# Kernel tuning notes

Hardware: AMD Instinct MI355X
Metric: run time of the kernel (lower is better)

Reference implementation:

```python
import math
import jax, jax.numpy as jnp
import numpy as np

CUTOFF = 5.0
NUM_RADIAL = 8   # num_basis_features
L_IN = 3         # basis_max_degree
L_OUT = 4        # moment_max_degree
F_OUT = 64       # num_moment_features


def _fact(n):
    return float(math.factorial(int(n)))


def _cg_complex(j1, j2, j3):
    """Clebsch-Gordan coefficients <j1 m1 j2 m2 | j3 m3> (Racah formula), complex SH basis."""
    C = np.zeros((2 * j1 + 1, 2 * j2 + 1, 2 * j3 + 1))
    for m1 in range(-j1, j1 + 1):
        for m2 in range(-j2, j2 + 1):
            m3 = m1 + m2
            if abs(m3) > j3:
                continue
            pref = math.sqrt((2 * j3 + 1) * _fact(j1 + j2 - j3) * _fact(j1 - j2 + j3)
                             * _fact(-j1 + j2 + j3) / _fact(j1 + j2 + j3 + 1))
            pref *= math.sqrt(_fact(j1 + m1) * _fact(j1 - m1) * _fact(j2 + m2)
                              * _fact(j2 - m2) * _fact(j3 + m3) * _fact(j3 - m3))
            kmin = max(0, j2 - j3 - m1, j1 - j3 + m2)
            kmax = min(j1 + j2 - j3, j1 - m1, j2 + m2)
            s = 0.0
            for k in range(kmin, kmax + 1):
                s += (-1) ** k / (_fact(k) * _fact(j1 + j2 - j3 - k) * _fact(j1 - m1 - k)
                                  * _fact(j2 + m2 - k) * _fact(j3 - j2 + m1 + k) * _fact(j3 - j1 - m2 + k))
            C[m1 + j1, m2 + j2, m3 + j3] = pref * s
    return C


def _u(l):
    """Unitary map complex SH -> real SH, m ordered -l..l."""
    U = np.zeros((2 * l + 1, 2 * l + 1), dtype=np.complex128)
    U[l, l] = 1.0
    for m in range(1, l + 1):
        U[l + m, l + m] = (-1) ** m / math.sqrt(2)
        U[l + m, l - m] = 1.0 / math.sqrt(2)
        U[l - m, l + m] = -1j * (-1) ** m / math.sqrt(2)
        U[l - m, l - m] = 1j / math.sqrt(2)
    return U


def _real_cg(l1, l2, l3):
    C = np.einsum('ai,bj,ck,ijk->abc', _u(l1), _u(l2), np.conj(_u(l3)), _cg_complex(l1, l2, l3))
    # parity-even paths (l1+l2+l3 even) are purely real in the real-SH basis
    return np.real(C).astype(np.float32)


# allowed coupling paths: triangle inequality + proper-tensor parity selection rule
PATHS = [(l1, l2, l3) for l1 in range(L_IN + 1) for l2 in range(L_IN + 1)
         for l3 in range(L_OUT + 1)
         if abs(l1 - l2) <= l3 <= l1 + l2 and (l1 + l2 + l3) % 2 == 0]
CG = {p: jnp.asarray(_real_cg(*p)) for p in PATHS}
OFF_IN = [0, 1, 4, 9, 16]  # degree-block offsets for max_degree=3


def _sph16(u):
    """Real orthonormal spherical harmonics l=0..3 on unit vectors, m=-l..l ordering."""
    x, y, z = u[..., 0], u[..., 1], u[..., 2]
    x2, y2, z2 = x * x, y * y, z * z
    Y = [
        0.28209479177387814 * jnp.ones_like(x),
        0.4886025119029199 * y, 0.4886025119029199 * z, 0.4886025119029199 * x,
        1.0925484305920792 * x * y, 1.0925484305920792 * y * z,
        0.31539156525252005 * (3.0 * z2 - 1.0),
        1.0925484305920792 * x * z, 0.5462742152960396 * (x2 - y2),
        0.5900435899266435 * y * (3.0 * x2 - y2), 2.890611442640554 * x * y * z,
        0.4570457994644658 * y * (5.0 * z2 - 1.0), 0.3731763325901154 * z * (5.0 * z2 - 3.0),
        0.4570457994644658 * x * (5.0 * z2 - 1.0), 1.445305721320277 * z * (x2 - y2),
        0.5900435899266435 * x * (x2 - 3.0 * y2),
    ]
    return jnp.stack(Y, axis=-1)


def _forward(disp, W1, W2):
    # disp: (N, M, 3)
    r = jnp.sqrt(jnp.sum(disp * disp, axis=-1) + 1e-12)          # (N, M)
    u = disp / r[..., None]
    Yang = _sph16(u)                                             # (N, M, 16)
    n = jnp.arange(1, NUM_RADIAL + 1, dtype=disp.dtype)
    radial = jnp.sinc(n * (r[..., None] / CUTOFF))               # sinc radial basis (N, M, 8)
    s2 = jnp.square(r / CUTOFF)
    inside = s2 < 1.0
    cut = jnp.where(inside, jnp.exp(1.0 - 1.0 / (1.0 - jnp.where(inside, s2, 0.0))), 0.0)
    basis = Yang[..., :, None] * (radial * cut[..., None])[..., None, :]   # (N, M, 16, 8)
    # TensorDense: two per-degree dense branches, then Clebsch-Gordan coupling
    y1 = [jnp.einsum('...mf,fg->...mg', basis[..., OFF_IN[l]:OFF_IN[l + 1], :], W1[l]) for l in range(L_IN + 1)]
    y2 = [jnp.einsum('...mf,fg->...mg', basis[..., OFF_IN[l]:OFF_IN[l + 1], :], W2[l]) for l in range(L_IN + 1)]
    out = [jnp.zeros(r.shape + (2 * l3 + 1, F_OUT), disp.dtype) for l3 in range(L_OUT + 1)]
    for (l1, l2, l3) in PATHS:
        out[l3] = out[l3] + jnp.einsum('...if,...jf,ijk->...kf', y1[l1], y2[l2], CG[(l1, l2, l3)])
    return jnp.concatenate(out, axis=-2)                         # (N, M, 25, 64)


def setup_inputs():
    key = jax.random.key(0)
    k1, k2, k3 = jax.random.split(key, 3)
    disp = 2.0 * jax.random.normal(k1, (4096, 16, 3), dtype=jnp.float32)
    W1 = jax.random.normal(k2, (4, 8, 64), dtype=jnp.float32) / math.sqrt(8.0)
    W2 = jax.random.normal(k3, (4, 8, 64), dtype=jnp.float32) / math.sqrt(8.0)
    return {"neighbour_displacements": disp, "W1": W1, "W2": W2}


def reference(neighbour_displacements, W1, W2):
    return _forward(neighbour_displacements, W1, W2)
```

## Files before the change

### kernel.cpp

```cpp
#include <hip/hip_runtime.h>
#include <cmath>
#include <complex>
#include <vector>
#include <algorithm>
#include <cstring>


#define MAXNNZ 4096

struct CGTab {
  int   rowPtr[136];
  int   ij[MAXNNZ];
  float co[MAXNNZ];
};

__device__ CGTab d_tab;


static double factd(int n) { double f = 1.0; for (int i = 2; i <= n; ++i) f *= (double)i; return f; }

static void cg_complex(int j1, int j2, int j3, std::vector<double>& C) {
  int d2 = 2 * j2 + 1, d3 = 2 * j3 + 1;
  C.assign((2 * j1 + 1) * d2 * d3, 0.0);
  for (int m1 = -j1; m1 <= j1; ++m1)
    for (int m2 = -j2; m2 <= j2; ++m2) {
      int m3 = m1 + m2;
      if (m3 < -j3 || m3 > j3) continue;
      double pref = std::sqrt((2 * j3 + 1) * factd(j1 + j2 - j3) * factd(j1 - j2 + j3) *
                              factd(-j1 + j2 + j3) / factd(j1 + j2 + j3 + 1));
      pref *= std::sqrt(factd(j1 + m1) * factd(j1 - m1) * factd(j2 + m2) *
                        factd(j2 - m2) * factd(j3 + m3) * factd(j3 - m3));
      int kmin = std::max(0, std::max(j2 - j3 - m1, j1 - j3 + m2));
      int kmax = std::min(j1 + j2 - j3, std::min(j1 - m1, j2 + m2));
      double s = 0.0;
      for (int k = kmin; k <= kmax; ++k) {
        s += ((k & 1) ? -1.0 : 1.0) /
             (factd(k) * factd(j1 + j2 - j3 - k) * factd(j1 - m1 - k) *
              factd(j2 + m2 - k) * factd(j3 - j2 + m1 + k) * factd(j3 - j1 - m2 + k));
      }
      C[((m1 + j1) * d2 + (m2 + j2)) * d3 + (m3 + j3)] = pref * s;
    }
}

static void umat(int l, std::vector<std::complex<double>>& U) {
  int d = 2 * l + 1;
  U.assign(d * d, std::complex<double>(0, 0));
  U[l * d + l] = 1.0;
  const double is2 = 1.0 / std::sqrt(2.0);
  for (int m = 1; m <= l; ++m) {
    double sg = (m & 1) ? -1.0 : 1.0;
    U[(l + m) * d + (l + m)] = sg * is2;
    U[(l + m) * d + (l - m)] = is2;
    U[(l - m) * d + (l + m)] = std::complex<double>(0, -sg * is2);
    U[(l - m) * d + (l - m)] = std::complex<double>(0, is2);
  }
}

static void real_cg(int l1, int l2, int l3, std::vector<double>& R) {
  std::vector<double> Cc;
  cg_complex(l1, l2, l3, Cc);
  std::vector<std::complex<double>> U1, U2, U3;
  umat(l1, U1); umat(l2, U2); umat(l3, U3);
  int d1 = 2 * l1 + 1, d2 = 2 * l2 + 1, d3 = 2 * l3 + 1;
  R.assign(d1 * d2 * d3, 0.0);
  for (int a = 0; a < d1; ++a)
    for (int b = 0; b < d2; ++b)
      for (int c = 0; c < d3; ++c) {
        std::complex<double> s(0, 0);
        for (int i = 0; i < d1; ++i)
          for (int j = 0; j < d2; ++j) {
            int k = (i - l1) + (j - l2) + l3;
            if (k < 0 || k >= d3) continue;
            double cc = Cc[(i * d2 + j) * d3 + k];
            if (cc == 0.0) continue;
            s += U1[a * d1 + i] * U2[b * d2 + j] * std::conj(U3[c * d3 + k]) * cc;
          }
        R[(a * d2 + b) * d3 + c] = s.real();
      }
}

static void build_tab(CGTab& T) {
  static const int off_in[5] = {0, 1, 4, 9, 16};
  int nnz = 0, slot = 0;
  std::vector<double> R;
  for (int l1 = 0; l1 <= 3; ++l1)
    for (int l2 = 0; l2 <= 3; ++l2)
      for (int l3 = 0; l3 <= 4; ++l3) {
        if (!(std::abs(l1 - l2) <= l3 && l3 <= l1 + l2 && ((l1 + l2 + l3) % 2 == 0))) continue;
        real_cg(l1, l2, l3, R);
        int d2 = 2 * l2 + 1, d3 = 2 * l3 + 1;
        for (int c = 0; c < d3; ++c) {
          T.rowPtr[slot] = nnz;
          for (int a = 0; a < 2 * l1 + 1; ++a)
            for (int b = 0; b < d2; ++b) {
              double v = R[(a * d2 + b) * d3 + c];
              if (std::fabs(v) > 1e-8 && nnz < MAXNNZ) {
                T.ij[nnz] = (off_in[l1] + a) | ((off_in[l2] + b) << 8);
                T.co[nnz] = (float)v;
                ++nnz;
              }
            }
          ++slot;
        }
      }
  T.rowPtr[slot] = nnz;
}


#define OUT_OFF(l3) ((l3) == 0 ? 0 : ((l3) == 1 ? 1 : ((l3) == 2 ? 4 : ((l3) == 3 ? 9 : 16))))

#define PATH(l1, l2, l3, sb)                                        \
  {                                                                 \
    const float t = R1v[l1] * R2v[l2];                              \
    _Pragma("unroll")                                               \
    for (int k = 0; k < 2 * (l3) + 1; ++k)                          \
      o[OUT_OFF(l3) + k] += t * Pl[(sb) + k];                       \
  }

__global__ __launch_bounds__(256) void atmd_kernel(
    const float* __restrict__ disp, const float* __restrict__ W1,
    const float* __restrict__ W2, float* __restrict__ out, int nE) {
  __shared__ float Ysh[4][16];
  __shared__ float P[4][136];

  const int tid = threadIdx.x;
  const int eL = tid >> 6;
  const int f = tid & 63;
  const int e = blockIdx.x * 4 + eL;
  const int ec = e < nE ? e : nE - 1;

  const float dx = disp[3 * ec + 0], dy = disp[3 * ec + 1], dz = disp[3 * ec + 2];
  const float r = sqrtf(dx * dx + dy * dy + dz * dz + 1e-12f);
  const float rinv = 1.0f / r;
  const float x = dx * rinv, y = dy * rinv, z = dz * rinv;
  const float x2 = x * x, y2 = y * y, z2 = z * z;

  const float s = r * 0.2f;
  const float s2 = s * s;
  const float cut = (s2 < 1.0f) ? expf(1.0f - 1.0f / (1.0f - s2)) : 0.0f;
  float radcut[8];
  const float PIF = 3.14159265358979323846f;
#pragma unroll
  for (int k = 0; k < 8; ++k) {
    float px = PIF * (float)(k + 1) * s;
    radcut[k] = cut * (sinf(px) / px);
  }

  if (f == 0) {
    float* q = &Ysh[eL][0];
    q[0]  = 0.28209479177387814f;
    q[1]  = 0.4886025119029199f * y;
    q[2]  = 0.4886025119029199f * z;
    q[3]  = 0.4886025119029199f * x;
    q[4]  = 1.0925484305920792f * x * y;
    q[5]  = 1.0925484305920792f * y * z;
    q[6]  = 0.31539156525252005f * (3.0f * z2 - 1.0f);
    q[7]  = 1.0925484305920792f * x * z;
    q[8]  = 0.5462742152960396f * (x2 - y2);
    q[9]  = 0.5900435899266435f * y * (3.0f * x2 - y2);
    q[10] = 2.890611442640554f * x * y * z;
    q[11] = 0.4570457994644658f * y * (5.0f * z2 - 1.0f);
    q[12] = 0.3731763325901154f * z * (5.0f * z2 - 3.0f);
    q[13] = 0.4570457994644658f * x * (5.0f * z2 - 1.0f);
    q[14] = 1.445305721320277f * z * (x2 - y2);
    q[15] = 0.5900435899266435f * x * (x2 - 3.0f * y2);
  }

  float R1v[4], R2v[4];
#pragma unroll
  for (int l = 0; l < 4; ++l) {
    float a = 0.f, b = 0.f;
#pragma unroll
    for (int k = 0; k < 8; ++k) {
      const float rc = radcut[k];
      a += rc * W1[(l * 8 + k) * 64 + f];
      b += rc * W2[(l * 8 + k) * 64 + f];
    }
    R1v[l] = a;
    R2v[l] = b;
  }

  __syncthreads();

  const float* Ye = &Ysh[eL][0];
  for (int sIdx = f; sIdx < 135; sIdx += 64) {
    const int b0 = d_tab.rowPtr[sIdx], b1 = d_tab.rowPtr[sIdx + 1];
    float acc = 0.f;
    for (int t = b0; t < b1; ++t) {
      const int p = d_tab.ij[t];
      acc += d_tab.co[t] * Ye[p & 255] * Ye[(p >> 8) & 255];
    }
    P[eL][sIdx] = acc;
  }
  __syncthreads();

  const float* Pl = &P[eL][0];
  float o[25];
#pragma unroll
  for (int k = 0; k < 25; ++k) o[k] = 0.f;

  PATH(0, 0, 0, 0)   PATH(0, 1, 1, 1)   PATH(0, 2, 2, 4)   PATH(0, 3, 3, 9)
  PATH(1, 0, 1, 16)  PATH(1, 1, 0, 19)  PATH(1, 1, 2, 20)  PATH(1, 2, 1, 25)
  PATH(1, 2, 3, 28)  PATH(1, 3, 2, 35)  PATH(1, 3, 4, 40)
  PATH(2, 0, 2, 49)  PATH(2, 1, 1, 54)  PATH(2, 1, 3, 57)  PATH(2, 2, 0, 64)
  PATH(2, 2, 2, 65)  PATH(2, 2, 4, 70)  PATH(2, 3, 1, 79)  PATH(2, 3, 3, 82)
  PATH(3, 0, 3, 89)  PATH(3, 1, 2, 96)  PATH(3, 1, 4, 101) PATH(3, 2, 1, 110)
  PATH(3, 2, 3, 113) PATH(3, 3, 0, 120) PATH(3, 3, 2, 121) PATH(3, 3, 4, 126)

  if (e < nE) {
    const size_t obase = (size_t)e * 1600 + f;
#pragma unroll
    for (int k3 = 0; k3 < 25; ++k3) out[obase + (size_t)k3 * 64] = o[k3];
  }
}


extern "C" void kernel_launch(void* const* d_in, const int* in_sizes, int n_in,
                              void* d_out, int out_size, void* d_ws, size_t ws_size,
                              hipStream_t stream) {
  const float* disp = (const float*)d_in[0];
  const float* W1 = (const float*)d_in[1];
  const float* W2 = (const float*)d_in[2];
  float* out = (float*)d_out;

  const int nE = in_sizes[0] / 3;

  static CGTab h_tab;
  build_tab(h_tab);
  void* sym = nullptr;
  (void)hipGetSymbolAddress(&sym, HIP_SYMBOL(d_tab));
  (void)hipMemcpyAsync(sym, &h_tab, sizeof(CGTab), hipMemcpyHostToDevice, stream);

  const int blocks = (nE + 3) / 4;
  atmd_kernel<<<blocks, 256, 0, stream>>>(disp, W1, W2, out, nE);
}
```

Before: 530.8 us.

## Split per-edge geometry and CG projection into separate kernel via workspace

Moves the spherical harmonics, radial basis and the sparse CG projection into a new edge kernel that spreads the 8 radial terms and 135 CG rows across threads and writes them to workspace. The feature kernel then reads these values back instead of recomputing the transcendental radial basis in all 64 feature lanes. The aim is to remove redundant per-lane sin/exp work and the serial CG loop from the output-bound kernel. In exchange it adds a second launch and a workspace round trip of about 144 floats per edge, and the edge kernel leaves many of its 160 threads per edge idle.

```diff
diff --git a/kernel.cpp b/kernel.cpp
--- a/kernel.cpp
+++ b/kernel.cpp
@@ -107,6 +107,63 @@
 }
 
 
+__global__ __launch_bounds__(320) void edge_kernel(
+    const float* __restrict__ disp, float* __restrict__ Pws,
+    float* __restrict__ RCws, int nE) {
+  __shared__ float Ysh[2][16];
+
+  const int tid = threadIdx.x;
+  const int half = (tid >= 160) ? 1 : 0;
+  const int slot = tid - half * 160;
+  const int e = blockIdx.x * 2 + half;
+
+  if (e < nE && slot <= 8) {
+    const float dx = disp[3 * e + 0], dy = disp[3 * e + 1], dz = disp[3 * e + 2];
+    const float r = sqrtf(dx * dx + dy * dy + dz * dz + 1e-12f);
+    if (slot < 8) {
+      const float s = r * 0.2f;
+      const float s2 = s * s;
+      const float cut = (s2 < 1.0f) ? expf(1.0f - 1.0f / (1.0f - s2)) : 0.0f;
+      const float px = 3.14159265358979323846f * (float)(slot + 1) * s;
+      RCws[e * 8 + slot] = cut * (sinf(px) / px);
+    } else {
+      const float rinv = 1.0f / r;
+      const float x = dx * rinv, y = dy * rinv, z = dz * rinv;
+      const float x2 = x * x, y2 = y * y, z2 = z * z;
+      float* q = &Ysh[half][0];
+      q[0]  = 0.28209479177387814f;
+      q[1]  = 0.4886025119029199f * y;
+      q[2]  = 0.4886025119029199f * z;
+      q[3]  = 0.4886025119029199f * x;
+      q[4]  = 1.0925484305920792f * x * y;
+      q[5]  = 1.0925484305920792f * y * z;
+      q[6]  = 0.31539156525252005f * (3.0f * z2 - 1.0f);
+      q[7]  = 1.0925484305920792f * x * z;
+      q[8]  = 0.5462742152960396f * (x2 - y2);
+      q[9]  = 0.5900435899266435f * y * (3.0f * x2 - y2);
+      q[10] = 2.890611442640554f * x * y * z;
+      q[11] = 0.4570457994644658f * y * (5.0f * z2 - 1.0f);
+      q[12] = 0.3731763325901154f * z * (5.0f * z2 - 3.0f);
+      q[13] = 0.4570457994644658f * x * (5.0f * z2 - 1.0f);
+      q[14] = 1.445305721320277f * z * (x2 - y2);
+      q[15] = 0.5900435899266435f * x * (x2 - 3.0f * y2);
+    }
+  }
+  __syncthreads();
+
+  if (e < nE && slot < 135) {
+    const int b0 = d_tab.rowPtr[slot], b1 = d_tab.rowPtr[slot + 1];
+    const float* Ye = &Ysh[half][0];
+    float acc = 0.f;
+    for (int t = b0; t < b1; ++t) {
+      const int p = d_tab.ij[t];
+      acc += d_tab.co[t] * Ye[p & 255] * Ye[(p >> 8) & 255];
+    }
+    Pws[(size_t)e * 136 + slot] = acc;
+  }
+}
+
+
 #define OUT_OFF(l3) ((l3) == 0 ? 0 : ((l3) == 1 ? 1 : ((l3) == 2 ? 4 : ((l3) == 3 ? 9 : 16))))
 
 #define PATH(l1, l2, l3, sb)                                        \
@@ -117,11 +174,12 @@
       o[OUT_OFF(l3) + k] += t * Pl[(sb) + k];                       \
   }
 
-__global__ __launch_bounds__(256) void atmd_kernel(
-    const float* __restrict__ disp, const float* __restrict__ W1,
-    const float* __restrict__ W2, float* __restrict__ out, int nE) {
-  __shared__ float Ysh[4][16];
+__global__ __launch_bounds__(256) void feat_kernel(
+    const float* __restrict__ W1, const float* __restrict__ W2,
+    const float* __restrict__ Pws, const float* __restrict__ RCws,
+    float* __restrict__ out, int nE) {
   __shared__ float P[4][136];
+  __shared__ float RC[4][8];
 
   const int tid = threadIdx.x;
   const int eL = tid >> 6;
@@ -129,42 +187,13 @@
   const int e = blockIdx.x * 4 + eL;
   const int ec = e < nE ? e : nE - 1;
 
-  const float dx = disp[3 * ec + 0], dy = disp[3 * ec + 1], dz = disp[3 * ec + 2];
-  const float r = sqrtf(dx * dx + dy * dy + dz * dz + 1e-12f);
-  const float rinv = 1.0f / r;
-  const float x = dx * rinv, y = dy * rinv, z = dz * rinv;
-  const float x2 = x * x, y2 = y * y, z2 = z * z;
-
-  const float s = r * 0.2f;
-  const float s2 = s * s;
-  const float cut = (s2 < 1.0f) ? expf(1.0f - 1.0f / (1.0f - s2)) : 0.0f;
-  float radcut[8];
-  const float PIF = 3.14159265358979323846f;
-#pragma unroll
-  for (int k = 0; k < 8; ++k) {
-    float px = PIF * (float)(k + 1) * s;
-    radcut[k] = cut * (sinf(px) / px);
-  }
-
-  if (f == 0) {
-    float* q = &Ysh[eL][0];
-    q[0]  = 0.28209479177387814f;
-    q[1]  = 0.4886025119029199f * y;
-    q[2]  = 0.4886025119029199f * z;
-    q[3]  = 0.4886025119029199f * x;
-    q[4]  = 1.0925484305920792f * x * y;
-    q[5]  = 1.0925484305920792f * y * z;
-    q[6]  = 0.31539156525252005f * (3.0f * z2 - 1.0f);
-    q[7]  = 1.0925484305920792f * x * z;
-    q[8]  = 0.5462742152960396f * (x2 - y2);
-    q[9]  = 0.5900435899266435f * y * (3.0f * x2 - y2);
-    q[10] = 2.890611442640554f * x * y * z;
-    q[11] = 0.4570457994644658f * y * (5.0f * z2 - 1.0f);
-    q[12] = 0.3731763325901154f * z * (5.0f * z2 - 3.0f);
-    q[13] = 0.4570457994644658f * x * (5.0f * z2 - 1.0f);
-    q[14] = 1.445305721320277f * z * (x2 - y2);
-    q[15] = 0.5900435899266435f * x * (x2 - 3.0f * y2);
-  }
+  for (int i = f; i < 135; i += 64) P[eL][i] = Pws[(size_t)ec * 136 + i];
+  if (f < 8) RC[eL][f] = RCws[ec * 8 + f];
+  __syncthreads();
+
+  float rc[8];
+#pragma unroll
+  for (int k = 0; k < 8; ++k) rc[k] = RC[eL][k];
 
   float R1v[4], R2v[4];
 #pragma unroll
@@ -172,27 +201,12 @@
     float a = 0.f, b = 0.f;
 #pragma unroll
     for (int k = 0; k < 8; ++k) {
-      const float rc = radcut[k];
-      a += rc * W1[(l * 8 + k) * 64 + f];
-      b += rc * W2[(l * 8 + k) * 64 + f];
+      a += rc[k] * W1[(l * 8 + k) * 64 + f];
+      b += rc[k] * W2[(l * 8 + k) * 64 + f];
     }
     R1v[l] = a;
     R2v[l] = b;
   }
-
-  __syncthreads();
-
-  const float* Ye = &Ysh[eL][0];
-  for (int sIdx = f; sIdx < 135; sIdx += 64) {
-    const int b0 = d_tab.rowPtr[sIdx], b1 = d_tab.rowPtr[sIdx + 1];
-    float acc = 0.f;
-    for (int t = b0; t < b1; ++t) {
-      const int p = d_tab.ij[t];
-      acc += d_tab.co[t] * Ye[p & 255] * Ye[(p >> 8) & 255];
-    }
-    P[eL][sIdx] = acc;
-  }
-  __syncthreads();
 
   const float* Pl = &P[eL][0];
   float o[25];
@@ -225,12 +239,15 @@
 
   const int nE = in_sizes[0] / 3;
 
+  float* Pws = (float*)d_ws;
+  float* RCws = Pws + (size_t)nE * 136;
+
   static CGTab h_tab;
   build_tab(h_tab);
   void* sym = nullptr;
   (void)hipGetSymbolAddress(&sym, HIP_SYMBOL(d_tab));
   (void)hipMemcpyAsync(sym, &h_tab, sizeof(CGTab), hipMemcpyHostToDevice, stream);
 
-  const int blocks = (nE + 3) / 4;
-  atmd_kernel<<<blocks, 256, 0, stream>>>(disp, W1, W2, out, nE);
-}
+  edge_kernel<<<(nE + 1) / 2, 320, 0, stream>>>(disp, Pws, RCws, nE);
+  feat_kernel<<<(nE + 3) / 4, 256, 0, stream>>>(W1, W2, Pws, RCws, out, nE);
+}
```

Result: slower. 555.6 us (+4.7%).

## Use a persistent grid with the CG table in LDS and stage output through LDS

Applied to the files above, without the earlier changes.

The kernel becomes persistent: a fixed grid of 2048 blocks loops over groups of 4 edges. Each block loads the CG sparse table into shared memory once as packed int2 pairs, and keeps its W1/W2 slices in registers. Radial basis values are computed once per edge by 8 lanes instead of by every thread. Output goes through a 25.6KB LDS buffer and is written back as coalesced float4 stores. Costs are one extra sync per group, rows padded to even length for a 2-way unrolled loop, and larger LDS use that may lower occupancy.

```diff
diff --git a/kernel.cpp b/kernel.cpp
--- a/kernel.cpp
+++ b/kernel.cpp
@@ -6,9 +6,12 @@
 #include <cstring>
 
 
-#define MAXNNZ 4096
+#define MAXNNZ 2048
+#define LDSNNZ 1536
+#define EPG 4
 
 struct CGTab {
+  int   nnzTotal;
   int   rowPtr[136];
   int   ij[MAXNNZ];
   float co[MAXNNZ];
@@ -100,10 +103,14 @@
                 ++nnz;
               }
             }
+          if ((nnz - T.rowPtr[slot]) & 1) {
+            if (nnz < MAXNNZ) { T.ij[nnz] = 0; T.co[nnz] = 0.0f; ++nnz; }
+          }
           ++slot;
         }
       }
   T.rowPtr[slot] = nnz;
+  T.nnzTotal = nnz;
 }
 
 
@@ -117,100 +124,136 @@
       o[OUT_OFF(l3) + k] += t * Pl[(sb) + k];                       \
   }
 
-__global__ __launch_bounds__(256) void atmd_kernel(
+__global__ __launch_bounds__(256) void atmd_fused(
     const float* __restrict__ disp, const float* __restrict__ W1,
-    const float* __restrict__ W2, float* __restrict__ out, int nE) {
-  __shared__ float Ysh[4][16];
-  __shared__ float P[4][136];
+    const float* __restrict__ W2, float* __restrict__ out,
+    int nE, int nGroups) {
+  __shared__ int2  Tab[LDSNNZ];
+  __shared__ int   RowP[136];
+  __shared__ float Ysh[EPG][16];
+  __shared__ float RCsh[EPG][8];
+  __shared__ float Rsh[EPG][2][4][64];
+  __shared__ float Psh[EPG][136];
+  __shared__ __align__(16) float Osh[EPG * 1600];
 
   const int tid = threadIdx.x;
-  const int eL = tid >> 6;
+  const int l = tid >> 6;
   const int f = tid & 63;
-  const int e = blockIdx.x * 4 + eL;
-  const int ec = e < nE ? e : nE - 1;
-
-  const float dx = disp[3 * ec + 0], dy = disp[3 * ec + 1], dz = disp[3 * ec + 2];
-  const float r = sqrtf(dx * dx + dy * dy + dz * dz + 1e-12f);
-  const float rinv = 1.0f / r;
-  const float x = dx * rinv, y = dy * rinv, z = dz * rinv;
-  const float x2 = x * x, y2 = y * y, z2 = z * z;
-
-  const float s = r * 0.2f;
-  const float s2 = s * s;
-  const float cut = (s2 < 1.0f) ? expf(1.0f - 1.0f / (1.0f - s2)) : 0.0f;
-  float radcut[8];
-  const float PIF = 3.14159265358979323846f;
+  const int eL = l;
+
+  const int nnz = d_tab.nnzTotal;
+  for (int t = tid; t < nnz; t += 256)
+    Tab[t] = make_int2(d_tab.ij[t], __float_as_int(d_tab.co[t]));
+  for (int t = tid; t < 136; t += 256) RowP[t] = d_tab.rowPtr[t];
+
+  float w1r[8], w2r[8];
 #pragma unroll
   for (int k = 0; k < 8; ++k) {
-    float px = PIF * (float)(k + 1) * s;
-    radcut[k] = cut * (sinf(px) / px);
-  }
-
-  if (f == 0) {
-    float* q = &Ysh[eL][0];
-    q[0]  = 0.28209479177387814f;
-    q[1]  = 0.4886025119029199f * y;
-    q[2]  = 0.4886025119029199f * z;
-    q[3]  = 0.4886025119029199f * x;
-    q[4]  = 1.0925484305920792f * x * y;
-    q[5]  = 1.0925484305920792f * y * z;
-    q[6]  = 0.31539156525252005f * (3.0f * z2 - 1.0f);
-    q[7]  = 1.0925484305920792f * x * z;
-    q[8]  = 0.5462742152960396f * (x2 - y2);
-    q[9]  = 0.5900435899266435f * y * (3.0f * x2 - y2);
-    q[10] = 2.890611442640554f * x * y * z;
-    q[11] = 0.4570457994644658f * y * (5.0f * z2 - 1.0f);
-    q[12] = 0.3731763325901154f * z * (5.0f * z2 - 3.0f);
-    q[13] = 0.4570457994644658f * x * (5.0f * z2 - 1.0f);
-    q[14] = 1.445305721320277f * z * (x2 - y2);
-    q[15] = 0.5900435899266435f * x * (x2 - 3.0f * y2);
-  }
-
-  float R1v[4], R2v[4];
-#pragma unroll
-  for (int l = 0; l < 4; ++l) {
-    float a = 0.f, b = 0.f;
-#pragma unroll
-    for (int k = 0; k < 8; ++k) {
-      const float rc = radcut[k];
-      a += rc * W1[(l * 8 + k) * 64 + f];
-      b += rc * W2[(l * 8 + k) * 64 + f];
-    }
-    R1v[l] = a;
-    R2v[l] = b;
-  }
-
-  __syncthreads();
-
-  const float* Ye = &Ysh[eL][0];
-  for (int sIdx = f; sIdx < 135; sIdx += 64) {
-    const int b0 = d_tab.rowPtr[sIdx], b1 = d_tab.rowPtr[sIdx + 1];
-    float acc = 0.f;
-    for (int t = b0; t < b1; ++t) {
-      const int p = d_tab.ij[t];
-      acc += d_tab.co[t] * Ye[p & 255] * Ye[(p >> 8) & 255];
-    }
-    P[eL][sIdx] = acc;
-  }
-  __syncthreads();
-
-  const float* Pl = &P[eL][0];
-  float o[25];
-#pragma unroll
-  for (int k = 0; k < 25; ++k) o[k] = 0.f;
-
-  PATH(0, 0, 0, 0)   PATH(0, 1, 1, 1)   PATH(0, 2, 2, 4)   PATH(0, 3, 3, 9)
-  PATH(1, 0, 1, 16)  PATH(1, 1, 0, 19)  PATH(1, 1, 2, 20)  PATH(1, 2, 1, 25)
-  PATH(1, 2, 3, 28)  PATH(1, 3, 2, 35)  PATH(1, 3, 4, 40)
-  PATH(2, 0, 2, 49)  PATH(2, 1, 1, 54)  PATH(2, 1, 3, 57)  PATH(2, 2, 0, 64)
-  PATH(2, 2, 2, 65)  PATH(2, 2, 4, 70)  PATH(2, 3, 1, 79)  PATH(2, 3, 3, 82)
-  PATH(3, 0, 3, 89)  PATH(3, 1, 2, 96)  PATH(3, 1, 4, 101) PATH(3, 2, 1, 110)
-  PATH(3, 2, 3, 113) PATH(3, 3, 0, 120) PATH(3, 3, 2, 121) PATH(3, 3, 4, 126)
-
-  if (e < nE) {
-    const size_t obase = (size_t)e * 1600 + f;
-#pragma unroll
-    for (int k3 = 0; k3 < 25; ++k3) out[obase + (size_t)k3 * 64] = o[k3];
+    w1r[k] = W1[(l * 8 + k) * 64 + f];
+    w2r[k] = W2[(l * 8 + k) * 64 + f];
+  }
+
+  for (int g = blockIdx.x; g < nGroups; g += gridDim.x) {
+    const int ebase = g * EPG;
+    __syncthreads();
+
+    const int e = ebase + eL;
+    if (f <= 8 && e < nE) {
+      const float dx = disp[3 * e + 0], dy = disp[3 * e + 1], dz = disp[3 * e + 2];
+      const float r = sqrtf(dx * dx + dy * dy + dz * dz + 1e-12f);
+      if (f >= 1) {
+        const float s = r * 0.2f;
+        const float s2 = s * s;
+        const float cutv = (s2 < 1.0f) ? expf(1.0f - 1.0f / (1.0f - s2)) : 0.0f;
+        const float px = 3.14159265358979323846f * (float)f * s;
+        RCsh[eL][f - 1] = cutv * (sinf(px) / px);
+      } else {
+        const float rinv = 1.0f / r;
+        const float x = dx * rinv, y = dy * rinv, z = dz * rinv;
+        const float x2 = x * x, y2 = y * y, z2 = z * z;
+        float* q = &Ysh[eL][0];
+        q[0]  = 0.28209479177387814f;
+        q[1]  = 0.4886025119029199f * y;
+        q[2]  = 0.4886025119029199f * z;
+        q[3]  = 0.4886025119029199f * x;
+        q[4]  = 1.0925484305920792f * x * y;
+        q[5]  = 1.0925484305920792f * y * z;
+        q[6]  = 0.31539156525252005f * (3.0f * z2 - 1.0f);
+        q[7]  = 1.0925484305920792f * x * z;
+        q[8]  = 0.5462742152960396f * (x2 - y2);
+        q[9]  = 0.5900435899266435f * y * (3.0f * x2 - y2);
+        q[10] = 2.890611442640554f * x * y * z;
+        q[11] = 0.4570457994644658f * y * (5.0f * z2 - 1.0f);
+        q[12] = 0.3731763325901154f * z * (5.0f * z2 - 3.0f);
+        q[13] = 0.4570457994644658f * x * (5.0f * z2 - 1.0f);
+        q[14] = 1.445305721320277f * z * (x2 - y2);
+        q[15] = 0.5900435899266435f * x * (x2 - 3.0f * y2);
+      }
+    }
+    __syncthreads();
+
+#pragma unroll
+    for (int e4 = 0; e4 < EPG; ++e4) {
+      float a = 0.f, b = 0.f;
+#pragma unroll
+      for (int k = 0; k < 8; ++k) {
+        const float rc = RCsh[e4][k];
+        a += rc * w1r[k];
+        b += rc * w2r[k];
+      }
+      Rsh[e4][0][l][f] = a;
+      Rsh[e4][1][l][f] = b;
+    }
+
+    for (int w = tid; w < EPG * 135; w += 256) {
+      const int e4 = w / 135;
+      const int s  = w - e4 * 135;
+      const int b0 = RowP[s], b1 = RowP[s + 1];
+      const float* Ye = &Ysh[e4][0];
+      float acc = 0.f;
+      for (int t = b0; t < b1; t += 2) {
+        const int2 en0 = Tab[t];
+        const int2 en1 = Tab[t + 1];
+        acc += __int_as_float(en0.y) * Ye[en0.x & 255] * Ye[(en0.x >> 8) & 255];
+        acc += __int_as_float(en1.y) * Ye[en1.x & 255] * Ye[(en1.x >> 8) & 255];
+      }
+      Psh[e4][s] = acc;
+    }
+    __syncthreads();
+
+    float R1v[4], R2v[4];
+#pragma unroll
+    for (int q = 0; q < 4; ++q) {
+      R1v[q] = Rsh[eL][0][q][f];
+      R2v[q] = Rsh[eL][1][q][f];
+    }
+    const float* Pl = &Psh[eL][0];
+    float o[25];
+#pragma unroll
+    for (int k = 0; k < 25; ++k) o[k] = 0.f;
+
+    PATH(0, 0, 0, 0)   PATH(0, 1, 1, 1)   PATH(0, 2, 2, 4)   PATH(0, 3, 3, 9)
+    PATH(1, 0, 1, 16)  PATH(1, 1, 0, 19)  PATH(1, 1, 2, 20)  PATH(1, 2, 1, 25)
+    PATH(1, 2, 3, 28)  PATH(1, 3, 2, 35)  PATH(1, 3, 4, 40)
+    PATH(2, 0, 2, 49)  PATH(2, 1, 1, 54)  PATH(2, 1, 3, 57)  PATH(2, 2, 0, 64)
+    PATH(2, 2, 2, 65)  PATH(2, 2, 4, 70)  PATH(2, 3, 1, 79)  PATH(2, 3, 3, 82)
+    PATH(3, 0, 3, 89)  PATH(3, 1, 2, 96)  PATH(3, 1, 4, 101) PATH(3, 2, 1, 110)
+    PATH(3, 2, 3, 113) PATH(3, 3, 0, 120) PATH(3, 3, 2, 121) PATH(3, 3, 4, 126)
+
+    {
+      float* Od = &Osh[eL * 1600 + f];
+#pragma unroll
+      for (int k3 = 0; k3 < 25; ++k3) Od[k3 * 64] = o[k3];
+    }
+    __syncthreads();
+
+    {
+      const int nvE = (nE - ebase) < EPG ? (nE - ebase) : EPG;
+      const int n4 = nvE * 400;
+      const float4* Os4 = (const float4*)Osh;
+      float4* out4 = (float4*)(out + (size_t)ebase * 1600);
+      for (int i = tid; i < n4; i += 256) out4[i] = Os4[i];
+    }
   }
 }
 
@@ -224,6 +267,7 @@
   float* out = (float*)d_out;
 
   const int nE = in_sizes[0] / 3;
+  const int nGroups = (nE + EPG - 1) / EPG;
 
   static CGTab h_tab;
   build_tab(h_tab);
@@ -231,6 +275,6 @@
   (void)hipGetSymbolAddress(&sym, HIP_SYMBOL(d_tab));
   (void)hipMemcpyAsync(sym, &h_tab, sizeof(CGTab), hipMemcpyHostToDevice, stream);
 
-  const int blocks = (nE + 3) / 4;
-  atmd_kernel<<<blocks, 256, 0, stream>>>(disp, W1, W2, out, nE);
-}
+  const int grid = 2048;
+  atmd_fused<<<grid, 256, 0, stream>>>(disp, W1, W2, out, nE, nGroups);
+}
```

After: 486.6 us. -8.3%, faster.
